# Kernel tuning notes

Measured on AMD Instinct MI355X. Metric: run time of the kernel, lower is better.

## Reference

```python
import jax, jax.numpy as jnp
import numpy as np

B, N, KNN_K, T_FRAC = 8, 4096, 32, 0.5
C_IN, C_OUT = 4, 64


def _knn_group(q, db, kk):
    """q: [Nq,3] queries, db: [Nd,3] database. Returns feats [Nq,kk,4], nn [Nq,kk,3]."""
    d2 = (jnp.sum(q * q, axis=-1, keepdims=True)
          + jnp.sum(db * db, axis=-1)[None, :]
          - 2.0 * (q @ db.T))                      # [Nq,Nd] squared dists
    _, idx = jax.lax.top_k(-d2, kk)                 # ascending distance, like pytorch3d knn_points
    nn = db[idx]                                    # [Nq,kk,3]
    resi = nn - q[:, None, :]                       # [Nq,kk,3]
    sq = jnp.sum(resi * resi, axis=-1, keepdims=True)
    dist = jnp.where(sq > 0, jnp.sqrt(jnp.where(sq > 0, sq, 1.0)), 0.0)  # safe norm (exact fwd)
    feats = jnp.concatenate([resi, dist], axis=-1)  # [Nq,kk,4]
    return feats, nn


def _forward(points1, points2, pc, Wq, Wk, Wv, bq, bk, bv, ridx1, ridx2, k, t):
    k2 = int(k * t)
    k1 = k - k2
    p1 = jnp.swapaxes(points1, 1, 2)  # [B,N,3]
    p2 = jnp.swapaxes(points2, 1, 2)
    p3 = jnp.swapaxes(pc, 1, 2)

    def per_batch(a, b, c, i1, i2):
        newp = jnp.concatenate([a[i1], b[i2]], axis=0)     # [N,3] fused candidate set
        f1, g1 = _knn_group(newp, a, k1)
        f2, g2 = _knn_group(newp, b, k2)
        f3, g3 = _knn_group(newp, c, k)
        feats = jnp.concatenate([f1, f2, f3], axis=1)      # [N,2k,4]
        grouped = jnp.concatenate([g1, g2, g3], axis=1)    # [N,2k,3]
        return feats, grouped

    feats, grouped = jax.vmap(per_batch)(p1, p2, p3, ridx1, ridx2)  # [B,N,2k,4], [B,N,2k,3]

    # SelfAttention over the neighbor axis (per point group)
    q = feats @ Wq + bq          # [B,N,2k,C_OUT]
    kf = feats @ Wk + bk
    v = feats @ Wv + bv
    scale = 1.0 / np.sqrt(C_OUT).astype(np.float32)
    attn = jax.nn.softmax(jnp.einsum('bnkc,bnjc->bnkj', q, kf) * scale, axis=-1)
    y = jnp.einsum('bnkj,bnjc->bnkc', attn, v)             # [B,N,2k,C_OUT]

    score = jnp.max(y, axis=-1)                            # max over channels -> [B,N,2k]
    w = jax.nn.softmax(score, axis=-1)                     # weights over 2k neighbors
    fused = jnp.einsum('bnk,bnkd->bdn', w, grouped)        # [B,3,N]
    return fused


def setup_inputs() -> dict:
    key = jax.random.key(0)
    ks = jax.random.split(key, 8)
    points1 = jax.random.normal(ks[0], (B, 3, N), dtype=jnp.float32)
    points2 = jax.random.normal(ks[1], (B, 3, N), dtype=jnp.float32)
    pc = jax.random.normal(ks[2], (B, 3, N), dtype=jnp.float32)
    N2 = int(N * T_FRAC)
    N1 = N - N2
    perm = lambda kk: jax.random.permutation(kk, N)
    ridx1 = jax.vmap(perm)(jax.random.split(ks[3], B))[:, :N1].astype(jnp.int32)
    ridx2 = jax.vmap(perm)(jax.random.split(ks[4], B))[:, :N2].astype(jnp.int32)
    s = 1.0 / np.sqrt(C_IN)
    Wq = jax.random.normal(ks[5], (C_IN, C_OUT), dtype=jnp.float32) * s
    Wk = jax.random.normal(ks[6], (C_IN, C_OUT), dtype=jnp.float32) * s
    Wv = jax.random.normal(ks[7], (C_IN, C_OUT), dtype=jnp.float32) * s
    z = jnp.zeros((C_OUT,), dtype=jnp.float32)
    return {"points1": points1, "points2": points2, "pc": pc,
            "Wq": Wq, "Wk": Wk, "Wv": Wv, "bq": z, "bk": z, "bv": z,
            "ridx1": ridx1, "ridx2": ridx2, "k": KNN_K, "t": T_FRAC}


def reference(points1, points2, pc, Wq, Wk, Wv, bq, bk, bv, ridx1, ridx2, k, t):
    return _forward(points1, points2, pc, Wq, Wk, Wv, bq, bk, bv, ridx1, ridx2, k, t)
```

## Files before the change

kernel.cpp:

```cpp
#include <hip/hip_runtime.h>
#include <hip/hip_bf16.h>
#include <math.h>

#define NB   8
#define NPT  4096
#define NQ1  2048
#define NQ2  2048
#define KTOT 64
#define TILE 1024
#define NTHR 256
#define QPB  128
#define TBUF 16
#define MPAD 33

#define PRM_OFF (4u << 20)

__global__ void pf2_setup(const float* __restrict__ Wq, const float* __restrict__ Wk,
                          const float* __restrict__ bq, const float* __restrict__ bk,
                          float* __restrict__ prm) {
    int t = threadIdx.x;
    const float sc = 0.125f;
    if (t < 16) {
        int p = t >> 2, q = t & 3;
        float a = 0.f;
        for (int c = 0; c < 64; ++c) a += Wq[p * 64 + c] * Wk[q * 64 + c];
        prm[t] = a * sc;
    } else if (t < 20) {
        int p = t - 16; float a = 0.f;
        for (int c = 0; c < 64; ++c) a += Wq[p * 64 + c] * bk[c];
        prm[t] = a * sc;
    } else if (t < 24) {
        int q = t - 20; float a = 0.f;
        for (int c = 0; c < 64; ++c) a += Wk[q * 64 + c] * bq[c];
        prm[t] = a * sc;
    } else if (t == 24) {
        float a = 0.f;
        for (int c = 0; c < 64; ++c) a += bq[c] * bk[c];
        prm[t] = a * sc;
    }
}

template <int K>
__device__ __forceinline__ void insert_med3(float (&dl)[K], int (&il)[K], float d, int id) {
    float pd = -INFINITY; int pi = 0;
    bool cp = false;
#pragma unroll
    for (int j = 0; j < K; ++j) {
        float oj = dl[j]; int ij = il[j];
        bool cj = d < oj;
        dl[j] = __builtin_amdgcn_fmed3f(d, pd, oj);
        il[j] = cp ? pi : (cj ? id : ij);
        pd = oj; pi = ij; cp = cj;
    }
}

template <int K>
__device__ void knn_half(const float* __restrict__ dbp,
                         float qx, float qy, float qz, int tid,
                         float4* __restrict__ tileLds,
                         unsigned short* __restrict__ bufLds,
                         float* __restrict__ mD,
                         unsigned short* __restrict__ mI,
                         unsigned short* __restrict__ outIdx) {
    const int q = tid & (QPB - 1), h = tid >> 7;
    float dl[K]; int il[K];
#pragma unroll
    for (int j = 0; j < K; ++j) { dl[j] = INFINITY; il[j] = 0; }
    float thresh = INFINITY;
    int cnt = 0;
    float4* tp = tileLds + h * TILE;

    for (int st = 0; st < 2; ++st) {
        int base = h * 2048 + st * TILE;
        __syncthreads();
        for (int r = 0; r < TILE / QPB; ++r) {
            int j = q + r * QPB;
            float x = dbp[base + j];
            float y = dbp[NPT + base + j];
            float z = dbp[2 * NPT + base + j];
            tp[j] = make_float4(-2.f * x, -2.f * y, -2.f * z,
                                fmaf(x, x, fmaf(y, y, z * z)));
        }
        __syncthreads();

        for (int c0 = 0; c0 < TILE; c0 += 8) {
            float sv[8];
#pragma unroll
            for (int u = 0; u < 8; ++u) {
                float4 p = tp[c0 + u];
                sv[u] = fmaf(p.x, qx, fmaf(p.y, qy, fmaf(p.z, qz, p.w)));
            }
#pragma unroll
            for (int u = 0; u < 8; ++u) {
                if (sv[u] < thresh) {
                    bufLds[cnt * NTHR + tid] = (unsigned short)(c0 + u);
                    ++cnt;
                }
            }
            if (__any(cnt > TBUF - 8)) {
                for (int u = 0; u < TBUF; ++u) {
                    if (!__any(u < cnt)) break;
                    if (u < cnt) {
                        int j = bufLds[u * NTHR + tid];
                        float4 p = tp[j];
                        float s = fmaf(p.x, qx, fmaf(p.y, qy, fmaf(p.z, qz, p.w)));
                        if (s < dl[K - 1]) insert_med3<K>(dl, il, s, base + j);
                    }
                }
                cnt = 0;
                thresh = dl[K - 1];
            }
        }
        for (int u = 0; u < TBUF; ++u) {
            if (!__any(u < cnt)) break;
            if (u < cnt) {
                int j = bufLds[u * NTHR + tid];
                float4 p = tp[j];
                float s = fmaf(p.x, qx, fmaf(p.y, qy, fmaf(p.z, qz, p.w)));
                if (s < dl[K - 1]) insert_med3<K>(dl, il, s, base + j);
            }
        }
        cnt = 0;
        thresh = dl[K - 1];
    }

    __syncthreads();
    if (h == 1) {
#pragma unroll
        for (int j = 0; j < K; ++j) {
            mD[q * MPAD + j] = dl[j];
            mI[q * MPAD + j] = (unsigned short)il[j];
        }
    }
    __syncthreads();
    if (h == 0) {
#pragma unroll
        for (int j = 0; j < K; ++j) {
            float d = mD[q * MPAD + j];
            int id = (int)mI[q * MPAD + j];
            if (d < dl[K - 1]) insert_med3<K>(dl, il, d, id);
        }
        unsigned* o32 = (unsigned*)outIdx;
#pragma unroll
        for (int u = 0; u < K / 2; ++u)
            o32[u] = (unsigned)(unsigned short)il[2 * u] |
                     ((unsigned)(unsigned short)il[2 * u + 1] << 16);
    }
}

__global__ __launch_bounds__(NTHR) void pf2_knn(const float* __restrict__ p1,
                                                const float* __restrict__ p2,
                                                const float* __restrict__ pc,
                                                const int* __restrict__ ridx1,
                                                const int* __restrict__ ridx2,
                                                unsigned short* __restrict__ wsIdx) {
    __shared__ float4 tileLds[2 * TILE];
    __shared__ unsigned short bufLds[TBUF * NTHR];
    float* mD = (float*)tileLds;
    unsigned short* mI = (unsigned short*)(mD + QPB * MPAD);

    int bid = blockIdx.x;
    int dbslot = bid >> 8;
    int db = (dbslot == 0) ? 2 : dbslot - 1;
    int rem = bid & 255;
    int b = rem >> 5;
    int chunk = rem & 31;
    int tid = threadIdx.x;
    int i = chunk * QPB + (tid & (QPB - 1));

    int j0; const float* srcp;
    if (i < NQ1) { j0 = ridx1[b * NQ1 + i]; srcp = p1; }
    else         { j0 = ridx2[b * NQ2 + (i - NQ1)]; srcp = p2; }
    const float* sb = srcp + (size_t)b * 3 * NPT;
    float qx = sb[j0], qy = sb[NPT + j0], qz = sb[2 * NPT + j0];

    const float* dbp = (db == 0 ? p1 : db == 1 ? p2 : pc) + (size_t)b * 3 * NPT;
    unsigned short* out = wsIdx + (size_t)(b * NPT + i) * KTOT +
                          (db == 0 ? 0 : db == 1 ? 16 : 32);
    if (db < 2) knn_half<16>(dbp, qx, qy, qz, tid, tileLds, bufLds, mD, mI, out);
    else        knn_half<32>(dbp, qx, qy, qz, tid, tileLds, bufLds, mD, mI, out);
}

__global__ __launch_bounds__(256) void pf2_attn(const float* __restrict__ p1,
                                                const float* __restrict__ p2,
                                                const float* __restrict__ pc,
                                                const int* __restrict__ ridx1,
                                                const int* __restrict__ ridx2,
                                                const float* __restrict__ Wv,
                                                const float* __restrict__ bv,
                                                const float* __restrict__ prm,
                                                const unsigned short* __restrict__ wsIdx,
                                                float* __restrict__ out) {
    __shared__ float4 wvt[64];
    __shared__ float  bvs[64];
    __shared__ float  prms[25];
    __shared__ float4 gl[4][64];
    __shared__ float4 fl[4][64];
    __shared__ float  sl[4][64];

    int tid = threadIdx.x;
    if (tid < 64) {
        wvt[tid] = make_float4(Wv[tid], Wv[64 + tid], Wv[128 + tid], Wv[192 + tid]);
        bvs[tid] = bv[tid];
    } else if (tid < 89) {
        prms[tid - 64] = prm[tid - 64];
    }
    __syncthreads();

    int wv = tid >> 6, lane = tid & 63;
    int g = blockIdx.x * 4 + wv;
    int b = g >> 12;
    int i = g & 4095;

    int j0; const float* srcp;
    if (i < NQ1) { j0 = ridx1[b * NQ1 + i]; srcp = p1; }
    else         { j0 = ridx2[b * NQ2 + (i - NQ1)]; srcp = p2; }
    const float* sb = srcp + (size_t)b * 3 * NPT;
    float qx = sb[j0], qy = sb[NPT + j0], qz = sb[2 * NPT + j0];

    int nidx = (int)wsIdx[(size_t)(b * NPT + i) * KTOT + lane];
    const float* dbp = (lane < 16 ? p1 : lane < 32 ? p2 : pc) + (size_t)b * 3 * NPT;
    float nx = dbp[nidx], ny = dbp[NPT + nidx], nz = dbp[2 * NPT + nidx];
    float fx = nx - qx, fy = ny - qy, fz = nz - qz;
    float sq = fx * fx + fy * fy + fz * fz;
    float fw = sq > 0.f ? sqrtf(sq) : 0.f;

    float gx = prms[0]  * fx + prms[1]  * fy + prms[2]  * fz + prms[3]  * fw;
    float gy = prms[4]  * fx + prms[5]  * fy + prms[6]  * fz + prms[7]  * fw;
    float gz = prms[8]  * fx + prms[9]  * fy + prms[10] * fz + prms[11] * fw;
    float gw = prms[12] * fx + prms[13] * fy + prms[14] * fz + prms[15] * fw;
    float sj = prms[20] * fx + prms[21] * fy + prms[22] * fz + prms[23] * fw;

    gl[wv][lane] = make_float4(gx, gy, gz, gw);
    fl[wv][lane] = make_float4(fx, fy, fz, fw);
    sl[wv][lane] = sj;
    __syncthreads();

    float m = -INFINITY;
    for (int j = 0; j < 64; ++j) {
        float4 gj = gl[wv][j];
        float l = fx * gj.x + fy * gj.y + fz * gj.z + fw * gj.w + sl[wv][j];
        m = fmaxf(m, l);
    }
    float S = 0.f, H0 = 0.f, H1 = 0.f, H2 = 0.f, H3 = 0.f;
    for (int j = 0; j < 64; ++j) {
        float4 gj = gl[wv][j];
        float4 fj = fl[wv][j];
        float l = fx * gj.x + fy * gj.y + fz * gj.z + fw * gj.w + sl[wv][j];
        float e = __expf(l - m);
        S += e;
        H0 += e * fj.x; H1 += e * fj.y; H2 += e * fj.z; H3 += e * fj.w;
    }
    float rS = 1.f / S;

    float smax = -INFINITY;
    for (int ch = 0; ch < 64; ++ch) {
        float4 wc = wvt[ch];
        float t = H0 * wc.x + H1 * wc.y + H2 * wc.z + H3 * wc.w;
        float yv = fmaf(t, rS, bvs[ch]);
        smax = fmaxf(smax, yv);
    }

    float M = smax;
    for (int off = 32; off; off >>= 1) M = fmaxf(M, __shfl_xor(M, off));
    float e = __expf(smax - M);
    float E = e;
    for (int off = 32; off; off >>= 1) E += __shfl_xor(E, off);
    float w = e / E;
    float px = w * nx, py = w * ny, pz = w * nz;
    for (int off = 32; off; off >>= 1) {
        px += __shfl_xor(px, off);
        py += __shfl_xor(py, off);
        pz += __shfl_xor(pz, off);
    }
    if (lane == 0) {
        float* ob = out + (size_t)b * 3 * NPT + i;
        ob[0] = px; ob[NPT] = py; ob[2 * NPT] = pz;
    }
}

extern "C" void kernel_launch(void* const* d_in, const int* in_sizes, int n_in,
                              void* d_out, int out_size, void* d_ws, size_t ws_size,
                              hipStream_t stream) {
    const float* p1 = (const float*)d_in[0];
    const float* p2 = (const float*)d_in[1];
    const float* pc = (const float*)d_in[2];
    const float* Wq = (const float*)d_in[3];
    const float* Wk = (const float*)d_in[4];
    const float* Wv = (const float*)d_in[5];
    const float* bq = (const float*)d_in[6];
    const float* bk = (const float*)d_in[7];
    const float* bv = (const float*)d_in[8];
    const int* ridx1 = (const int*)d_in[9];
    const int* ridx2 = (const int*)d_in[10];
    float* out = (float*)d_out;

    unsigned short* wsIdx = (unsigned short*)d_ws;
    float* prm = (float*)((char*)d_ws + PRM_OFF);

    pf2_setup<<<1, 32, 0, stream>>>(Wq, Wk, bq, bk, prm);
    pf2_knn<<<NB * 3 * (NPT / QPB), NTHR, 0, stream>>>(p1, p2, pc, ridx1, ridx2, wsIdx);
    pf2_attn<<<NB * NPT / 4, 256, 0, stream>>>(p1, p2, pc, ridx1, ridx2, Wv, bv, prm, wsIdx, out);
}
```

Before: 377.7 us.

## Split KNN into distance-only selection pass and index-recovery second pass

The KNN selection now runs in two passes. The first keeps only sorted distances, buffering distance values and using a cheaper med3 insert with no index tracking. The second re-streams the database tile and recovers indices by matching candidates at or below the final threshold against the stored distances. The merge buffer layout also changes from padded row-major to column-major. The cost is loading and scanning the tiles twice, plus a possible tie-handling difference when equal distances occur.

```diff
diff --git a/kernel.cpp b/kernel.cpp
--- a/kernel.cpp
+++ b/kernel.cpp
@@ -11,7 +11,6 @@
 #define NTHR 256
 #define QPB  128
 #define TBUF 16
-#define MPAD 33
 
 #define PRM_OFF (4u << 20)
 
@@ -58,19 +57,38 @@
 __device__ void knn_half(const float* __restrict__ dbp,
                          float qx, float qy, float qz, int tid,
                          float4* __restrict__ tileLds,
-                         unsigned short* __restrict__ bufLds,
+                         unsigned* __restrict__ dbuf,
                          float* __restrict__ mD,
                          unsigned short* __restrict__ mI,
                          unsigned short* __restrict__ outIdx) {
     const int q = tid & (QPB - 1), h = tid >> 7;
-    float dl[K]; int il[K];
-#pragma unroll
-    for (int j = 0; j < K; ++j) { dl[j] = INFINITY; il[j] = 0; }
+    float4* tp = tileLds + h * TILE;
+    unsigned short* ibuf = (unsigned short*)dbuf;
+
+    float dl[K];
+#pragma unroll
+    for (int j = 0; j < K; ++j) dl[j] = INFINITY;
     float thresh = INFINITY;
     int cnt = 0;
-    float4* tp = tileLds + h * TILE;
-
-    for (int st = 0; st < 2; ++st) {
+
+    auto flushD = [&]() {
+        for (int u = 0; u < TBUF; ++u) {
+            if (!__any(u < cnt)) break;
+            unsigned bits = dbuf[u * NTHR + tid];
+            float s = (u < cnt) ? __uint_as_float(bits) : INFINITY;
+            float pd = -INFINITY;
+#pragma unroll
+            for (int j = 0; j < K; ++j) {
+                float oj = dl[j];
+                dl[j] = __builtin_amdgcn_fmed3f(s, pd, oj);
+                pd = oj;
+            }
+        }
+        cnt = 0;
+        thresh = dl[K - 1];
+    };
+
+    for (int st = 0; st < 2048 / TILE; ++st) {
         int base = h * 2048 + st * TILE;
         __syncthreads();
         for (int r = 0; r < TILE / QPB; ++r) {
@@ -93,58 +111,97 @@
 #pragma unroll
             for (int u = 0; u < 8; ++u) {
                 if (sv[u] < thresh) {
-                    bufLds[cnt * NTHR + tid] = (unsigned short)(c0 + u);
+                    dbuf[cnt * NTHR + tid] = __float_as_uint(sv[u]);
                     ++cnt;
                 }
             }
-            if (__any(cnt > TBUF - 8)) {
-                for (int u = 0; u < TBUF; ++u) {
-                    if (!__any(u < cnt)) break;
-                    if (u < cnt) {
-                        int j = bufLds[u * NTHR + tid];
-                        float4 p = tp[j];
-                        float s = fmaf(p.x, qx, fmaf(p.y, qy, fmaf(p.z, qz, p.w)));
-                        if (s < dl[K - 1]) insert_med3<K>(dl, il, s, base + j);
-                    }
-                }
-                cnt = 0;
-                thresh = dl[K - 1];
-            }
-        }
+            if (__any(cnt > TBUF - 8)) flushD();
+        }
+    }
+    flushD();
+    const float mt = dl[K - 1];
+
+    int il[K];
+#pragma unroll
+    for (int j = 0; j < K; ++j) il[j] = -1;
+
+    auto flushM = [&](int base) {
         for (int u = 0; u < TBUF; ++u) {
             if (!__any(u < cnt)) break;
-            if (u < cnt) {
-                int j = bufLds[u * NTHR + tid];
-                float4 p = tp[j];
-                float s = fmaf(p.x, qx, fmaf(p.y, qy, fmaf(p.z, qz, p.w)));
-                if (s < dl[K - 1]) insert_med3<K>(dl, il, s, base + j);
+            bool act = (u < cnt);
+            int j = act ? (int)ibuf[u * NTHR + tid] : 0;
+            float4 p = tp[j];
+            float s = fmaf(p.x, qx, fmaf(p.y, qy, fmaf(p.z, qz, p.w)));
+            if (!act) s = INFINITY;
+            int idx = base + j;
+            bool placed = false;
+#pragma unroll
+            for (int jj = 0; jj < K; ++jj) {
+                bool take = (!placed) && (il[jj] < 0) && (s == dl[jj]);
+                il[jj] = take ? idx : il[jj];
+                placed = placed || take;
             }
         }
         cnt = 0;
-        thresh = dl[K - 1];
+    };
+
+    cnt = 0;
+    for (int st = 0; st < 2048 / TILE; ++st) {
+        int base = h * 2048 + st * TILE;
+        __syncthreads();
+        for (int r = 0; r < TILE / QPB; ++r) {
+            int j = q + r * QPB;
+            float x = dbp[base + j];
+            float y = dbp[NPT + base + j];
+            float z = dbp[2 * NPT + base + j];
+            tp[j] = make_float4(-2.f * x, -2.f * y, -2.f * z,
+                                fmaf(x, x, fmaf(y, y, z * z)));
+        }
+        __syncthreads();
+
+        for (int c0 = 0; c0 < TILE; c0 += 8) {
+            float sv[8];
+#pragma unroll
+            for (int u = 0; u < 8; ++u) {
+                float4 p = tp[c0 + u];
+                sv[u] = fmaf(p.x, qx, fmaf(p.y, qy, fmaf(p.z, qz, p.w)));
+            }
+#pragma unroll
+            for (int u = 0; u < 8; ++u) {
+                if (sv[u] <= mt) {
+                    ibuf[cnt * NTHR + tid] = (unsigned short)(c0 + u);
+                    ++cnt;
+                }
+            }
+            if (__any(cnt > TBUF - 8)) flushM(base);
+        }
+        flushM(base);
     }
 
     __syncthreads();
     if (h == 1) {
 #pragma unroll
         for (int j = 0; j < K; ++j) {
-            mD[q * MPAD + j] = dl[j];
-            mI[q * MPAD + j] = (unsigned short)il[j];
+            mD[j * QPB + q] = dl[j];
+            mI[j * QPB + q] = (unsigned short)il[j];
         }
     }
     __syncthreads();
     if (h == 0) {
+        int ilo[K]; float dlo[K];
+#pragma unroll
+        for (int j = 0; j < K; ++j) { dlo[j] = dl[j]; ilo[j] = il[j]; }
 #pragma unroll
         for (int j = 0; j < K; ++j) {
-            float d = mD[q * MPAD + j];
-            int id = (int)mI[q * MPAD + j];
-            if (d < dl[K - 1]) insert_med3<K>(dl, il, d, id);
+            float d = mD[j * QPB + q];
+            int id = (int)mI[j * QPB + q];
+            if (d < dlo[K - 1]) insert_med3<K>(dlo, ilo, d, id);
         }
         unsigned* o32 = (unsigned*)outIdx;
 #pragma unroll
         for (int u = 0; u < K / 2; ++u)
-            o32[u] = (unsigned)(unsigned short)il[2 * u] |
-                     ((unsigned)(unsigned short)il[2 * u + 1] << 16);
+            o32[u] = (unsigned)(unsigned short)ilo[2 * u] |
+                     ((unsigned)(unsigned short)ilo[2 * u + 1] << 16);
     }
 }
 
@@ -155,9 +212,9 @@
                                                 const int* __restrict__ ridx2,
                                                 unsigned short* __restrict__ wsIdx) {
     __shared__ float4 tileLds[2 * TILE];
-    __shared__ unsigned short bufLds[TBUF * NTHR];
+    __shared__ unsigned dbuf[TBUF * NTHR];
     float* mD = (float*)tileLds;
-    unsigned short* mI = (unsigned short*)(mD + QPB * MPAD);
+    unsigned short* mI = (unsigned short*)(mD + 32 * QPB);
 
     int bid = blockIdx.x;
     int dbslot = bid >> 8;
@@ -177,8 +234,8 @@
     const float* dbp = (db == 0 ? p1 : db == 1 ? p2 : pc) + (size_t)b * 3 * NPT;
     unsigned short* out = wsIdx + (size_t)(b * NPT + i) * KTOT +
                           (db == 0 ? 0 : db == 1 ? 16 : 32);
-    if (db < 2) knn_half<16>(dbp, qx, qy, qz, tid, tileLds, bufLds, mD, mI, out);
-    else        knn_half<32>(dbp, qx, qy, qz, tid, tileLds, bufLds, mD, mI, out);
+    if (db < 2) knn_half<16>(dbp, qx, qy, qz, tid, tileLds, dbuf, mD, mI, out);
+    else        knn_half<32>(dbp, qx, qy, qz, tid, tileLds, dbuf, mD, mI, out);
 }
 
 __global__ __launch_bounds__(256) void pf2_attn(const float* __restrict__ p1,
```

Measured after the change: 431.8 us. +14.3%, slower.
